# Kernel optimization log

Measured on AMD Instinct MI355X. Metric: run time of the kernel, lower is better.

## Reference

```python
import jax, jax.numpy as jnp
import numpy as np

NH, DH, BS, HS = 8, 16, 8, 3           # heads, head dim, block size, halo size
WIN = BS + 2 * HS                      # 14
DIM, DIM_V = 256, 256
SCALE = DH ** -0.5


def setup_inputs() -> dict:
    key = jax.random.key(0)
    k1, k2, k3, k4, k5 = jax.random.split(key, 5)
    x = jax.random.normal(k1, (8, DIM, 64, 64), jnp.float32)
    q_w = jax.random.normal(k2, (NH * DH, DIM), jnp.float32) * (DIM ** -0.5)
    kv_w = jax.random.normal(k3, (NH * DH + DIM_V, DIM), jnp.float32) * (DIM ** -0.5)
    height_rel = jax.random.normal(k4, (2 * WIN - 1, DH), jnp.float32) * SCALE
    width_rel = jax.random.normal(k5, (2 * WIN - 1, DH), jnp.float32) * SCALE
    return {"x": x, "q_w": q_w, "kv_w": kv_w, "height_rel": height_rel, "width_rel": width_rel}


def _rel_logits_1d(q, rel_k, perm):
    N, Hq, Wq, d = q.shape
    rel_size = rel_k.shape[0]
    win = (rel_size + 1) // 2
    x = jnp.einsum('nhwd,rd->nhwr', q, rel_k).reshape(N * Hq, Wq, rel_size)
    x = jnp.pad(x, ((0, 0), (0, 0), (0, 1))).reshape(N * Hq, Wq * (rel_size + 1))
    x = jnp.pad(x, ((0, 0), (0, rel_size - Wq))).reshape(N * Hq, Wq + 1, rel_size)
    x = x[:, :Wq, win - 1:]
    x = jnp.broadcast_to(x.reshape(N, Hq, 1, Wq, win), (N, Hq, win, Wq, win))
    return x.transpose(perm)


def _pos_embed(q, height_rel, width_rel):
    Bh, nb, HW, dh = q.shape
    qb = q.reshape(-1, BS, BS, dh)
    rw = _rel_logits_1d(qb, width_rel, (0, 1, 3, 2, 4))
    rh = _rel_logits_1d(qb.transpose(0, 2, 1, 3), height_rel, (0, 3, 1, 4, 2))
    return (rh + rw).reshape(Bh, nb, HW, -1)


def reference(x, q_w, kv_w, height_rel, width_rel):
    B, C, H, W = x.shape
    nHb, nWb = H // BS, W // BS
    nb = nHb * nWb
    dvh = DIM_V // NH

    # q: 1x1 conv + block-unfold -> (B*nh, nb, bs*bs, dh)
    q = jnp.einsum('bchw,oc->bohw', x, q_w)
    q = q.reshape(B, NH, DH, nHb, BS, nWb, BS).transpose(0, 1, 3, 5, 4, 6, 2)
    q = q.reshape(B * NH, nb, BS * BS, DH)

    kv = jnp.einsum('bchw,oc->bohw', x, kv_w)
    kvp = jnp.pad(kv, ((0, 0), (0, 0), (HS, HS), (HS, HS)))
    rows = jnp.arange(nHb)[:, None] * BS + jnp.arange(WIN)[None, :]
    cols = jnp.arange(nWb)[:, None] * BS + jnp.arange(WIN)[None, :]
    wins = kvp[:, :, rows][:, :, :, :, cols]
    wins = wins.transpose(0, 1, 2, 4, 3, 5)
    wins = wins.reshape(B, NH, DH + dvh, nb, WIN * WIN).transpose(0, 1, 3, 4, 2)
    wins = wins.reshape(B * NH, nb, WIN * WIN, DH + dvh)
    k, v = wins[..., :DH], wins[..., DH:]

    attn = jnp.einsum('znqd,znkd->znqk', q, k) * SCALE + _pos_embed(q, height_rel, width_rel)
    attn = jax.nn.softmax(attn, axis=-1)
    out = jnp.einsum('znqk,znkd->znqd', attn, v)        # (B*nh, nb, bs*bs, dvh)

    # fold blocks back to (B, dim_v, H, W)
    out = out.reshape(B, NH, nHb, nWb, BS, BS, dvh).transpose(0, 1, 6, 2, 4, 3, 5)
    return out.reshape(B, DIM_V, H, W)
```

## Files before the change

### kernel.cpp

```cpp
#include <hip/hip_runtime.h>
#include <hip/hip_bf16.h>

#define LOG2E 1.4426950408889634f

typedef __attribute__((ext_vector_type(8))) short bf16x8;
typedef __attribute__((ext_vector_type(4))) float f32x4;
typedef __attribute__((ext_vector_type(16))) float f32x16;

__device__ __forceinline__ short f2bf(float a) {
  __hip_bfloat16 h = __float2bfloat16(a);
  return *reinterpret_cast<short*>(&h);
}
__device__ __forceinline__ unsigned pkbf(float a, float b) {
  return (unsigned)(unsigned short)f2bf(a) | ((unsigned)(unsigned short)f2bf(b) << 16);
}
__device__ __forceinline__ unsigned cvtpk(float a, float b) {
  unsigned r;
  asm("v_cvt_pk_bf16_f32 %0, %1, %2" : "=v"(r) : "v"(a), "v"(b));
  return r;
}
__device__ __forceinline__ float bfu2f(unsigned u16v) {
  unsigned v = u16v << 16; float f; __builtin_memcpy(&f, &v, 4); return f;
}
union FragU8 { unsigned d[4]; bf16x8 v; };
union KU { uint4 u; bf16x8 v; };

__global__ __launch_bounds__(256) void haloattn_cvt(
    const float* __restrict__ x, const float* __restrict__ q_w,
    const float* __restrict__ kv_w, unsigned short* __restrict__ xT,
    unsigned short* __restrict__ w_bf)
{
  __shared__ float Ld[64][68];
  const int t = threadIdx.x;
  const int pt = blockIdx.x, kt = blockIdx.y, b = blockIdx.z;
  {
    const int flat = ((b << 2) + kt) * 64 + pt;
    const int idx = flat * 64 + (t & 63);
    if (t < 64) {
      const float wv = (idx < 32768) ? q_w[idx] : kv_w[idx - 32768];
      w_bf[idx] = (unsigned short)f2bf(wv);
    }
  }
  const float* xb = x + ((size_t)b * 256 + (kt << 6)) * 4096 + (pt << 6);
#pragma unroll
  for (int ps = 0; ps < 4; ++ps) {
    const int kloc = (ps << 4) + (t >> 4);
    const int ploc = (t & 15) << 2;
    float4 v = *(const float4*)(xb + (size_t)kloc * 4096 + ploc);
    *(float4*)&Ld[kloc][ploc] = v;
  }
  __syncthreads();
  const int pl = t >> 2;
  const int ks = (t & 3) << 4;
  float f[16];
#pragma unroll
  for (int i = 0; i < 16; ++i) f[i] = Ld[ks + i][pl];
  uint4 o0, o1;
  o0.x = pkbf(f[0], f[1]);   o0.y = pkbf(f[2], f[3]);
  o0.z = pkbf(f[4], f[5]);   o0.w = pkbf(f[6], f[7]);
  o1.x = pkbf(f[8], f[9]);   o1.y = pkbf(f[10], f[11]);
  o1.z = pkbf(f[12], f[13]); o1.w = pkbf(f[14], f[15]);
  unsigned short* op = xT + ((size_t)(b << 12) + (pt << 6) + pl) * 256 + (kt << 6) + ks;
  *(uint4*)op = o0;
  *(uint4*)(op + 8) = o1;
}

__global__ __launch_bounds__(512, 4) void haloattn_proj_mfma(
    const unsigned short* __restrict__ xT, const unsigned short* __restrict__ w_bf,
    unsigned short* __restrict__ q_bf, unsigned short* __restrict__ kbuf,
    unsigned short* __restrict__ vpln)
{
  __shared__ unsigned short Wt[256][68];
  __shared__ unsigned short Xt[128][68];
  const int tid = threadIdx.x;
  const int w = tid >> 6, l = tid & 63;
  const int b = blockIdx.z, oBase = blockIdx.y << 8, pBase = blockIdx.x << 7;
  const int wm = w >> 1, wn = w & 1;
  const int g = l >> 4, c = l & 15;

  f32x4 acc[4][4] = {};

  const int srow = tid >> 3;
  const int se3  = (tid & 7) << 3;

  for (int chk = 0; chk < 4; ++chk) {
    const int k0 = chk << 6;
#pragma unroll
    for (int ps = 0; ps < 4; ++ps) {
      const int row = (ps << 6) + srow;
      uint4 wv = *(const uint4*)(w_bf + (size_t)(oBase + row) * 256 + k0 + se3);
      char* dst = (char*)&Wt[0][0] + row * 136 + (se3 << 1);
      *(uint2*)dst = make_uint2(wv.x, wv.y);
      *(uint2*)(dst + 8) = make_uint2(wv.z, wv.w);
    }
#pragma unroll
    for (int ps = 0; ps < 2; ++ps) {
      const int p = (ps << 6) + srow;
      uint4 xv = *(const uint4*)(xT + ((size_t)(b << 12) + pBase + p) * 256 + k0 + se3);
      char* dst = (char*)&Xt[0][0] + p * 136 + (se3 << 1);
      *(uint2*)dst = make_uint2(xv.x, xv.y);
      *(uint2*)(dst + 8) = make_uint2(xv.z, xv.w);
    }
    __syncthreads();
#pragma unroll
    for (int kk = 0; kk < 2; ++kk) {
      FragU8 bfr[4];
#pragma unroll
      for (int nf = 0; nf < 4; ++nf) {
        const char* src = (const char*)&Xt[0][0]
            + ((wn << 6) + (nf << 4) + c) * 136 + (kk << 6) + (g << 4);
        uint2 lo = *(const uint2*)src, hi2 = *(const uint2*)(src + 8);
        bfr[nf].d[0] = lo.x; bfr[nf].d[1] = lo.y;
        bfr[nf].d[2] = hi2.x; bfr[nf].d[3] = hi2.y;
      }
#pragma unroll
      for (int mf = 0; mf < 4; ++mf) {
        const char* src = (const char*)&Wt[0][0]
            + ((wm << 6) + (mf << 4) + c) * 136 + (kk << 6) + (g << 4);
        uint2 lo = *(const uint2*)src, hi2 = *(const uint2*)(src + 8);
        FragU8 af;
        af.d[0] = lo.x; af.d[1] = lo.y; af.d[2] = hi2.x; af.d[3] = hi2.y;
#pragma unroll
        for (int nf = 0; nf < 4; ++nf)
          acc[mf][nf] = __builtin_amdgcn_mfma_f32_16x16x32_bf16(af.v, bfr[nf].v, acc[mf][nf], 0, 0, 0);
      }
    }
    __syncthreads();
  }
#pragma unroll
  for (int mf = 0; mf < 4; ++mf) {
    const int o = oBase + (wm << 6) + (mf << 4) + (g << 2);
#pragma unroll
    for (int nf = 0; nf < 4; ++nf) {
      const int p = pBase + (wn << 6) + (nf << 4) + c;
      if (o < 128) {
        uint2 pk2 = make_uint2(pkbf(acc[mf][nf][0], acc[mf][nf][1]),
                               pkbf(acc[mf][nf][2], acc[mf][nf][3]));
        const int head = o >> 4;
        const int z = (b << 3) + head;
        const int y = p >> 6, xx = p & 63;
        const int nbb = ((y >> 3) << 3) + (xx >> 3);
        const int qi = ((y & 7) << 3) + (xx & 7);
        *(uint2*)(q_bf + (((size_t)z * 64 + nbb) * 64 + qi) * 16 + (o & 15)) = pk2;
      } else {
        const int ch = o - 128;
        const int head = (ch * 1366) >> 16;
        const int wi = ch - head * 48;
        const int b8h = (b << 3) + head;
        if (wi < 16) {
          uint2 pk2 = make_uint2(pkbf(acc[mf][nf][0], acc[mf][nf][1]),
                                 pkbf(acc[mf][nf][2], acc[mf][nf][3]));
          *(uint2*)(kbuf + ((size_t)b8h * 4096 + p) * 16 + wi) = pk2;
        } else {
          const int d = wi - 16;
          const int y = p >> 6, xx = p & 63;
          unsigned short* vp = vpln + (size_t)(b8h * 32 + d) * 5040
                               + (size_t)(y + 3) * 72 + (xx + 3);
          vp[0]     = (unsigned short)f2bf(acc[mf][nf][0]);
          vp[5040]  = (unsigned short)f2bf(acc[mf][nf][1]);
          vp[10080] = (unsigned short)f2bf(acc[mf][nf][2]);
          vp[15120] = (unsigned short)f2bf(acc[mf][nf][3]);
        }
      }
    }
  }
}

__global__ __launch_bounds__(64, 2) void haloattn_attn_direct(
    const unsigned short* __restrict__ q_bf, const unsigned short* __restrict__ kbuf,
    const unsigned short* __restrict__ vpln,
    const float* __restrict__ height_rel, const float* __restrict__ width_rel,
    float* __restrict__ out)
{
  __shared__ __align__(16) unsigned short SM[5376];

  const int l = threadIdx.x;
  const int q32 = l & 31, hi = l >> 5;
  const int wg = blockIdx.x;
  const int swz = ((wg & 7) << 9) | (wg >> 3);
  const int z = swz >> 6;
  const int nb = swz & 63;
  const int b = z >> 3, head = z & 7;
  const int bi = nb >> 3, bj = nb & 7;
  const int swapA = (l ^ 32) << 2;
  const f32x16 z16 = {};
  const float qs = 0.25f * LOG2E;

  const unsigned short* qtile = q_bf + ((size_t)z * 64 + nb) * 1024;
  bf16x8 qfrag[2];
  qfrag[0] = *(const bf16x8*)(qtile + q32 * 16 + 8 * hi);
  qfrag[1] = *(const bf16x8*)(qtile + (32 + q32) * 16 + 8 * hi);

  unsigned short* HRs = SM;
  unsigned short* WRs = SM + 768;
  if (l < 54) {
    const int u = l >> 1, d0 = (l & 1) << 3;
    float4 a = *(const float4*)(height_rel + u * 16 + d0);
    float4 b4 = *(const float4*)(height_rel + u * 16 + d0 + 4);
    uint4 o;
    o.x = cvtpk(a.x * LOG2E, a.y * LOG2E);
    o.y = cvtpk(a.z * LOG2E, a.w * LOG2E);
    o.z = cvtpk(b4.x * LOG2E, b4.y * LOG2E);
    o.w = cvtpk(b4.z * LOG2E, b4.w * LOG2E);
    *(uint4*)(HRs + u * 24 + d0) = o;
    a = *(const float4*)(width_rel + u * 16 + d0);
    b4 = *(const float4*)(width_rel + u * 16 + d0 + 4);
    o.x = cvtpk(a.x * LOG2E, a.y * LOG2E);
    o.y = cvtpk(a.z * LOG2E, a.w * LOG2E);
    o.z = cvtpk(b4.x * LOG2E, b4.y * LOG2E);
    o.w = cvtpk(b4.z * LOG2E, b4.w * LOG2E);
    *(uint4*)(WRs + u * 24 + d0) = o;
  } else {
    const int t = l - 54;
    const int u = 27 + (t >> 1), d0 = (t & 1) << 3;
    uint4 o = {};
    *(uint4*)(HRs + u * 24 + d0) = o;
    *(uint4*)(WRs + u * 24 + d0) = o;
  }
  __syncthreads();

  {
    bf16x8 hfr = *(const bf16x8*)((const char*)HRs + q32 * 48 + 16 * hi);
    bf16x8 wfr = *(const bf16x8*)((const char*)WRs + q32 * 48 + 16 * hi);
    f32x16 h0 = __builtin_amdgcn_mfma_f32_32x32x16_bf16(hfr, qfrag[0], z16, 0, 0, 0);
    f32x16 h1 = __builtin_amdgcn_mfma_f32_32x32x16_bf16(hfr, qfrag[1], z16, 0, 0, 0);
    f32x16 w0 = __builtin_amdgcn_mfma_f32_32x32x16_bf16(wfr, qfrag[0], z16, 0, 0, 0);
    f32x16 w1 = __builtin_amdgcn_mfma_f32_32x32x16_bf16(wfr, qfrag[1], z16, 0, 0, 0);
    __syncthreads();
#pragma unroll
    for (int r = 0; r < 16; ++r) {
      const int u = (r & 3) + 8 * (r >> 2) + 4 * hi;
      if (u >= 6 && u < 27) {
        const int rr = u - 6;
        SM[rr * 64 + q32]               = (unsigned short)f2bf(h0[r]);
        SM[(21 + rr) * 64 + q32]        = (unsigned short)f2bf(h1[r]);
        SM[2688 + rr * 64 + q32]        = (unsigned short)f2bf(w0[r]);
        SM[2688 + (21 + rr) * 64 + q32] = (unsigned short)f2bf(w1[r]);
      }
    }
  }
  __syncthreads();

  const int qw = q32 & 7;
  float wreg[2][8];
#pragma unroll
  for (int nt = 0; nt < 2; ++nt)
#pragma unroll
    for (int t = 0; t < 8; ++t) {
      const int jt = (t < 4 ? t : t + 4) + 4 * hi;
      if (jt < 14)
        wreg[nt][t] = bfu2f(SM[2688 + (nt * 21 + 7 - qw + jt) * 64 + q32]);
      else
        wreg[nt][t] = -1e30f;
    }

  const int qh0 = q32 >> 3;
  const unsigned short* Hp0 = SM + (7 - qh0) * 64 + q32;
  const unsigned short* Hp1 = SM + (24 - qh0) * 64 + q32;

  const int jj = q32 & 15, ir = q32 >> 4;
  const int xx = bj * 8 + jj - 3;
  const bool jok = (jj < 14) && ((unsigned)xx < 64u);
  const unsigned short* kb = kbuf + ((size_t)((b << 3) + head) * 4096 + xx) * 16 + 8 * hi;
  const int yy0 = bi * 8 + ir - 3;
  const unsigned short* vb = vpln + (size_t)(((b << 3) + head) * 32 + q32) * 5040
                             + (bi * 8) * 72 + bj * 8 + 8 * hi;

  f32x16 acc[2] = {};
  float lrow[2] = {0.f, 0.f};

  KU k4; k4.u = make_uint4(0, 0, 0, 0);
  if (jok && (unsigned)yy0 < 64u) k4.u = *(const uint4*)(kb + (size_t)yy0 * 1024);
  bf16x8 v0n = *(const bf16x8*)(vb);
  bf16x8 v1n = *(const bf16x8*)(vb + 72);

  for (int c = 0; c < 7; ++c) {
    const bf16x8 kf = k4.v;
    const bf16x8 vf0 = v0n, vf1 = v1n;
    if (c < 6) {
      const int yy = yy0 + 2 * (c + 1);
      KU kn; kn.u = make_uint4(0, 0, 0, 0);
      if (jok && (unsigned)yy < 64u) kn.u = *(const uint4*)(kb + (size_t)yy * 1024);
      k4 = kn;
      v0n = *(const bf16x8*)(vb + (2 * c + 2) * 72);
      v1n = *(const bf16x8*)(vb + (2 * c + 3) * 72);
    }
#pragma unroll
    for (int nt = 0; nt < 2; ++nt) {
      f32x16 Cs = __builtin_amdgcn_mfma_f32_32x32x16_bf16(kf, qfrag[nt], z16, 0, 0, 0);
      const unsigned short* Hp = nt ? Hp1 : Hp0;
      const float hA = bfu2f(Hp[(2 * c) * 64]);
      const float hB = bfu2f(Hp[(2 * c + 1) * 64]);
      float p[16];
#pragma unroll
      for (int r = 0; r < 16; ++r) {
        const float wv = wreg[nt][(r & 3) + 4 * ((r >> 2) & 1)];
        const float h = (r < 8) ? hA : hB;
        p[r] = exp2f(fmaf(Cs[r], qs, h + wv));
      }
      {
        float s0 = (p[0] + p[1]) + (p[2] + p[3]);
        float s1 = (p[4] + p[5]) + (p[6] + p[7]);
        float s2 = (p[8] + p[9]) + (p[10] + p[11]);
        float s3 = (p[12] + p[13]) + (p[14] + p[15]);
        lrow[nt] += (s0 + s1) + (s2 + s3);
      }
      unsigned dw[8], xw[8];
#pragma unroll
      for (int k = 0; k < 8; ++k) dw[k] = cvtpk(p[2 * k], p[2 * k + 1]);
#pragma unroll
      for (int k = 0; k < 8; ++k)
        xw[k] = (unsigned)__builtin_amdgcn_ds_bpermute(swapA, (int)dw[k]);
      FragU8 f0, f1;
      f0.d[0] = hi ? xw[2] : dw[0];
      f0.d[1] = hi ? xw[3] : dw[1];
      f0.d[2] = hi ? dw[2] : xw[0];
      f0.d[3] = hi ? dw[3] : xw[1];
      f1.d[0] = hi ? xw[6] : dw[4];
      f1.d[1] = hi ? xw[7] : dw[5];
      f1.d[2] = hi ? dw[6] : xw[4];
      f1.d[3] = hi ? dw[7] : xw[5];
      acc[nt] = __builtin_amdgcn_mfma_f32_32x32x16_bf16(vf0, f0.v, acc[nt], 0, 0, 0);
      acc[nt] = __builtin_amdgcn_mfma_f32_32x32x16_bf16(vf1, f1.v, acc[nt], 0, 0, 0);
    }
  }

#pragma unroll
  for (int nt = 0; nt < 2; ++nt) {
    const float L = lrow[nt] + __shfl_xor(lrow[nt], 32);
    const float invL = 1.f / L;
    const int qt = nt * 32 + q32;
    const int yq = bi * 8 + (qt >> 3);
    const int xq = bj * 8 + (q32 & 7);
    float* obase = out + ((size_t)(b * 256 + head * 32) * 4096) + yq * 64 + xq;
#pragma unroll
    for (int r = 0; r < 16; ++r) {
      const int d = (r & 3) + 8 * (r >> 2) + 4 * hi;
      obase[(size_t)d * 4096] = acc[nt][r] * invL;
    }
  }
}

extern "C" void kernel_launch(void* const* d_in, const int* in_sizes, int n_in,
                              void* d_out, int out_size, void* d_ws, size_t ws_size,
                              hipStream_t stream) {
  const float* x          = (const float*)d_in[0];
  const float* q_w        = (const float*)d_in[1];
  const float* kv_w       = (const float*)d_in[2];
  const float* height_rel = (const float*)d_in[3];
  const float* width_rel  = (const float*)d_in[4];
  float* out = (float*)d_out;

  unsigned short* q_bf = (unsigned short*)d_ws;
  unsigned short* xT   = q_bf + (size_t)4194304;
  unsigned short* w_bf = xT + (size_t)8388608;
  unsigned short* kbuf = w_bf + (size_t)131072;
  unsigned short* vpln = kbuf + (size_t)4194304;

  hipMemsetAsync(vpln, 0, (size_t)10321920 * 2, stream);
  haloattn_cvt<<<dim3(64, 4, 8), 256, 0, stream>>>(x, q_w, kv_w, xT, w_bf);
  haloattn_proj_mfma<<<dim3(32, 2, 8), 512, 0, stream>>>(xT, w_bf, q_bf, kbuf, vpln);
  haloattn_attn_direct<<<4096, 64, 0, stream>>>(q_bf, kbuf, vpln,
                                                height_rel, width_rel, out);
}
```

Before: 77.26 us.

## Split attention work across two waves and zero only halo borders in cvt

Result: faster. 66.29 us (-14.2%).

```diff
diff --git a/kernel.cpp b/kernel.cpp
--- a/kernel.cpp
+++ b/kernel.cpp
@@ -28,17 +28,34 @@
 __global__ __launch_bounds__(256) void haloattn_cvt(
     const float* __restrict__ x, const float* __restrict__ q_w,
     const float* __restrict__ kv_w, unsigned short* __restrict__ xT,
-    unsigned short* __restrict__ w_bf)
+    unsigned short* __restrict__ w_bf, unsigned short* __restrict__ vpln)
 {
   __shared__ float Ld[64][68];
   const int t = threadIdx.x;
   const int pt = blockIdx.x, kt = blockIdx.y, b = blockIdx.z;
+  const int flat = ((b << 2) + kt) * 64 + pt;
   {
-    const int flat = ((b << 2) + kt) * 64 + pt;
     const int idx = flat * 64 + (t & 63);
     if (t < 64) {
       const float wv = (idx < 32768) ? q_w[idx] : kv_w[idx - 32768];
       w_bf[idx] = (unsigned short)f2bf(wv);
+    }
+  }
+  {
+    unsigned short* pl = vpln + (size_t)flat * 5040;
+    for (int e = t; e < 944; e += 256) {
+      int off;
+      if (e < 216) {
+        off = e;
+      } else if (e < 432) {
+        off = 4824 + (e - 216);
+      } else {
+        const int tt = e - 432;
+        const int y = 3 + (tt >> 3);
+        const int cidx = tt & 7;
+        off = y * 72 + (cidx < 3 ? cidx : cidx + 64);
+      }
+      pl[off] = 0;
     }
   }
   const float* xb = x + ((size_t)b * 256 + (kt << 6)) * 4096 + (pt << 6);
@@ -166,7 +183,7 @@
   }
 }
 
-__global__ __launch_bounds__(64, 2) void haloattn_attn_direct(
+__global__ __launch_bounds__(128, 2) void haloattn_attn_direct(
     const unsigned short* __restrict__ q_bf, const unsigned short* __restrict__ kbuf,
     const unsigned short* __restrict__ vpln,
     const float* __restrict__ height_rel, const float* __restrict__ width_rel,
@@ -174,7 +191,9 @@
 {
   __shared__ __align__(16) unsigned short SM[5376];
 
-  const int l = threadIdx.x;
+  const int tid = threadIdx.x;
+  const int w = tid >> 6;
+  const int l = tid & 63;
   const int q32 = l & 31, hi = l >> 5;
   const int wg = blockIdx.x;
   const int swz = ((wg & 7) << 9) | (wg >> 3);
@@ -187,14 +206,12 @@
   const float qs = 0.25f * LOG2E;
 
   const unsigned short* qtile = q_bf + ((size_t)z * 64 + nb) * 1024;
-  bf16x8 qfrag[2];
-  qfrag[0] = *(const bf16x8*)(qtile + q32 * 16 + 8 * hi);
-  qfrag[1] = *(const bf16x8*)(qtile + (32 + q32) * 16 + 8 * hi);
+  const bf16x8 qfrag = *(const bf16x8*)(qtile + (((w << 5) + q32) << 4) + 8 * hi);
 
   unsigned short* HRs = SM;
   unsigned short* WRs = SM + 768;
-  if (l < 54) {
-    const int u = l >> 1, d0 = (l & 1) << 3;
+  if (tid < 54) {
+    const int u = tid >> 1, d0 = (tid & 1) << 3;
     float4 a = *(const float4*)(height_rel + u * 16 + d0);
     float4 b4 = *(const float4*)(height_rel + u * 16 + d0 + 4);
     uint4 o;
@@ -210,8 +227,8 @@
     o.z = cvtpk(b4.x * LOG2E, b4.y * LOG2E);
     o.w = cvtpk(b4.z * LOG2E, b4.w * LOG2E);
     *(uint4*)(WRs + u * 24 + d0) = o;
-  } else {
-    const int t = l - 54;
+  } else if (tid < 64) {
+    const int t = tid - 54;
     const int u = 27 + (t >> 1), d0 = (t & 1) << 3;
     uint4 o = {};
     *(uint4*)(HRs + u * 24 + d0) = o;
@@ -222,41 +239,34 @@
   {
     bf16x8 hfr = *(const bf16x8*)((const char*)HRs + q32 * 48 + 16 * hi);
     bf16x8 wfr = *(const bf16x8*)((const char*)WRs + q32 * 48 + 16 * hi);
-    f32x16 h0 = __builtin_amdgcn_mfma_f32_32x32x16_bf16(hfr, qfrag[0], z16, 0, 0, 0);
-    f32x16 h1 = __builtin_amdgcn_mfma_f32_32x32x16_bf16(hfr, qfrag[1], z16, 0, 0, 0);
-    f32x16 w0 = __builtin_amdgcn_mfma_f32_32x32x16_bf16(wfr, qfrag[0], z16, 0, 0, 0);
-    f32x16 w1 = __builtin_amdgcn_mfma_f32_32x32x16_bf16(wfr, qfrag[1], z16, 0, 0, 0);
+    f32x16 hC = __builtin_amdgcn_mfma_f32_32x32x16_bf16(hfr, qfrag, z16, 0, 0, 0);
+    f32x16 wC = __builtin_amdgcn_mfma_f32_32x32x16_bf16(wfr, qfrag, z16, 0, 0, 0);
     __syncthreads();
 #pragma unroll
     for (int r = 0; r < 16; ++r) {
       const int u = (r & 3) + 8 * (r >> 2) + 4 * hi;
       if (u >= 6 && u < 27) {
-        const int rr = u - 6;
-        SM[rr * 64 + q32]               = (unsigned short)f2bf(h0[r]);
-        SM[(21 + rr) * 64 + q32]        = (unsigned short)f2bf(h1[r]);
-        SM[2688 + rr * 64 + q32]        = (unsigned short)f2bf(w0[r]);
-        SM[2688 + (21 + rr) * 64 + q32] = (unsigned short)f2bf(w1[r]);
+        const int rr = (w * 21) + (u - 6);
+        SM[rr * 64 + q32]        = (unsigned short)f2bf(hC[r]);
+        SM[2688 + rr * 64 + q32] = (unsigned short)f2bf(wC[r]);
       }
     }
   }
   __syncthreads();
 
   const int qw = q32 & 7;
-  float wreg[2][8];
-#pragma unroll
-  for (int nt = 0; nt < 2; ++nt)
-#pragma unroll
-    for (int t = 0; t < 8; ++t) {
-      const int jt = (t < 4 ? t : t + 4) + 4 * hi;
-      if (jt < 14)
-        wreg[nt][t] = bfu2f(SM[2688 + (nt * 21 + 7 - qw + jt) * 64 + q32]);
-      else
-        wreg[nt][t] = -1e30f;
-    }
+  float wreg[8];
+#pragma unroll
+  for (int t = 0; t < 8; ++t) {
+    const int jt = (t < 4 ? t : t + 4) + 4 * hi;
+    if (jt < 14)
+      wreg[t] = bfu2f(SM[2688 + (w * 21 + 7 - qw + jt) * 64 + q32]);
+    else
+      wreg[t] = -1e30f;
+  }
 
   const int qh0 = q32 >> 3;
-  const unsigned short* Hp0 = SM + (7 - qh0) * 64 + q32;
-  const unsigned short* Hp1 = SM + (24 - qh0) * 64 + q32;
+  const unsigned short* Hp = SM + ((w ? 24 : 7) - qh0) * 64 + q32;
 
   const int jj = q32 & 15, ir = q32 >> 4;
   const int xx = bj * 8 + jj - 3;
@@ -266,8 +276,8 @@
   const unsigned short* vb = vpln + (size_t)(((b << 3) + head) * 32 + q32) * 5040
                              + (bi * 8) * 72 + bj * 8 + 8 * hi;
 
-  f32x16 acc[2] = {};
-  float lrow[2] = {0.f, 0.f};
+  f32x16 acc = {};
+  float lrow = 0.f;
 
   KU k4; k4.u = make_uint4(0, 0, 0, 0);
   if (jok && (unsigned)yy0 < 64u) k4.u = *(const uint4*)(kb + (size_t)yy0 * 1024);
@@ -285,59 +295,56 @@
       v0n = *(const bf16x8*)(vb + (2 * c + 2) * 72);
       v1n = *(const bf16x8*)(vb + (2 * c + 3) * 72);
     }
-#pragma unroll
-    for (int nt = 0; nt < 2; ++nt) {
-      f32x16 Cs = __builtin_amdgcn_mfma_f32_32x32x16_bf16(kf, qfrag[nt], z16, 0, 0, 0);
-      const unsigned short* Hp = nt ? Hp1 : Hp0;
-      const float hA = bfu2f(Hp[(2 * c) * 64]);
-      const float hB = bfu2f(Hp[(2 * c + 1) * 64]);
-      float p[16];
-#pragma unroll
-      for (int r = 0; r < 16; ++r) {
-        const float wv = wreg[nt][(r & 3) + 4 * ((r >> 2) & 1)];
-        const float h = (r < 8) ? hA : hB;
-        p[r] = exp2f(fmaf(Cs[r], qs, h + wv));
-      }
-      {
-        float s0 = (p[0] + p[1]) + (p[2] + p[3]);
-        float s1 = (p[4] + p[5]) + (p[6] + p[7]);
-        float s2 = (p[8] + p[9]) + (p[10] + p[11]);
-        float s3 = (p[12] + p[13]) + (p[14] + p[15]);
-        lrow[nt] += (s0 + s1) + (s2 + s3);
-      }
-      unsigned dw[8], xw[8];
-#pragma unroll
-      for (int k = 0; k < 8; ++k) dw[k] = cvtpk(p[2 * k], p[2 * k + 1]);
-#pragma unroll
-      for (int k = 0; k < 8; ++k)
-        xw[k] = (unsigned)__builtin_amdgcn_ds_bpermute(swapA, (int)dw[k]);
-      FragU8 f0, f1;
-      f0.d[0] = hi ? xw[2] : dw[0];
-      f0.d[1] = hi ? xw[3] : dw[1];
-      f0.d[2] = hi ? dw[2] : xw[0];
-      f0.d[3] = hi ? dw[3] : xw[1];
-      f1.d[0] = hi ? xw[6] : dw[4];
-      f1.d[1] = hi ? xw[7] : dw[5];
-      f1.d[2] = hi ? dw[6] : xw[4];
-      f1.d[3] = hi ? dw[7] : xw[5];
-      acc[nt] = __builtin_amdgcn_mfma_f32_32x32x16_bf16(vf0, f0.v, acc[nt], 0, 0, 0);
-      acc[nt] = __builtin_amdgcn_mfma_f32_32x32x16_bf16(vf1, f1.v, acc[nt], 0, 0, 0);
-    }
-  }
-
-#pragma unroll
-  for (int nt = 0; nt < 2; ++nt) {
-    const float L = lrow[nt] + __shfl_xor(lrow[nt], 32);
-    const float invL = 1.f / L;
-    const int qt = nt * 32 + q32;
-    const int yq = bi * 8 + (qt >> 3);
-    const int xq = bj * 8 + (q32 & 7);
-    float* obase = out + ((size_t)(b * 256 + head * 32) * 4096) + yq * 64 + xq;
+    __builtin_amdgcn_s_setprio(1);
+    f32x16 Cs = __builtin_amdgcn_mfma_f32_32x32x16_bf16(kf, qfrag, z16, 0, 0, 0);
+    __builtin_amdgcn_s_setprio(0);
+    const float hA = bfu2f(Hp[(2 * c) * 64]);
+    const float hB = bfu2f(Hp[(2 * c + 1) * 64]);
+    float p[16];
 #pragma unroll
     for (int r = 0; r < 16; ++r) {
-      const int d = (r & 3) + 8 * (r >> 2) + 4 * hi;
-      obase[(size_t)d * 4096] = acc[nt][r] * invL;
-    }
+      const float wv = wreg[(r & 3) + 4 * ((r >> 2) & 1)];
+      const float h = (r < 8) ? hA : hB;
+      p[r] = exp2f(fmaf(Cs[r], qs, h + wv));
+    }
+    {
+      float s0 = (p[0] + p[1]) + (p[2] + p[3]);
+      float s1 = (p[4] + p[5]) + (p[6] + p[7]);
+      float s2 = (p[8] + p[9]) + (p[10] + p[11]);
+      float s3 = (p[12] + p[13]) + (p[14] + p[15]);
+      lrow += (s0 + s1) + (s2 + s3);
+    }
+    unsigned dw[8], xw[8];
+#pragma unroll
+    for (int k = 0; k < 8; ++k) dw[k] = cvtpk(p[2 * k], p[2 * k + 1]);
+#pragma unroll
+    for (int k = 0; k < 8; ++k)
+      xw[k] = (unsigned)__builtin_amdgcn_ds_bpermute(swapA, (int)dw[k]);
+    FragU8 f0, f1;
+    f0.d[0] = hi ? xw[2] : dw[0];
+    f0.d[1] = hi ? xw[3] : dw[1];
+    f0.d[2] = hi ? dw[2] : xw[0];
+    f0.d[3] = hi ? dw[3] : xw[1];
+    f1.d[0] = hi ? xw[6] : dw[4];
+    f1.d[1] = hi ? xw[7] : dw[5];
+    f1.d[2] = hi ? dw[6] : xw[4];
+    f1.d[3] = hi ? dw[7] : xw[5];
+    __builtin_amdgcn_s_setprio(1);
+    acc = __builtin_amdgcn_mfma_f32_32x32x16_bf16(vf0, f0.v, acc, 0, 0, 0);
+    acc = __builtin_amdgcn_mfma_f32_32x32x16_bf16(vf1, f1.v, acc, 0, 0, 0);
+    __builtin_amdgcn_s_setprio(0);
+  }
+
+  const float L = lrow + __shfl_xor(lrow, 32);
+  const float invL = 1.f / L;
+  const int qt = (w << 5) + q32;
+  const int yq = bi * 8 + (qt >> 3);
+  const int xq = bj * 8 + (q32 & 7);
+  float* obase = out + ((size_t)(b * 256 + head * 32) * 4096) + yq * 64 + xq;
+#pragma unroll
+  for (int r = 0; r < 16; ++r) {
+    const int d = (r & 3) + 8 * (r >> 2) + 4 * hi;
+    obase[(size_t)d * 4096] = acc[r] * invL;
   }
 }
 
@@ -357,9 +364,8 @@
   unsigned short* kbuf = w_bf + (size_t)131072;
   unsigned short* vpln = kbuf + (size_t)4194304;
 
-  hipMemsetAsync(vpln, 0, (size_t)10321920 * 2, stream);
-  haloattn_cvt<<<dim3(64, 4, 8), 256, 0, stream>>>(x, q_w, kv_w, xT, w_bf);
+  haloattn_cvt<<<dim3(64, 4, 8), 256, 0, stream>>>(x, q_w, kv_w, xT, w_bf, vpln);
   haloattn_proj_mfma<<<dim3(32, 2, 8), 512, 0, stream>>>(xT, w_bf, q_bf, kbuf, vpln);
-  haloattn_attn_direct<<<4096, 64, 0, stream>>>(q_bf, kbuf, vpln,
-                                                height_rel, width_rel, out);
-}
+  haloattn_attn_direct<<<4096, 128, 0, stream>>>(q_bf, kbuf, vpln,
+                                                 height_rel, width_rel, out);
+}
```
